# Kernel optimization log

Hardware: AMD Instinct MI355X
Metric: run time of the kernel (lower is better)

The kernel has to match this reference:

```python
import jax, jax.numpy as jnp
import numpy as np

EPS = 1e-5
N = 384
CZ = 128  # pair channels (c_z)
CH = 128  # hidden channels (c_hidden)


def _layer_norm(x, w, b):
    m = jnp.mean(x, axis=-1, keepdims=True)
    v = jnp.mean(jnp.square(x - m), axis=-1, keepdims=True)
    return (x - m) * jax.lax.rsqrt(v + EPS) * w + b


def setup_inputs() -> dict:
    key = jax.random.key(0)
    ks = jax.random.split(key, 8)
    s = 0.02  # weight init scale
    return {
        "z": jax.random.normal(ks[0], (1, N, N, CZ), jnp.float32),
        "ln_in_w": jnp.ones((2, CZ), jnp.float32),
        "ln_in_b": jnp.zeros((2, CZ), jnp.float32),
        "w_ag": jax.random.normal(ks[1], (2, CZ, CH), jnp.float32) * s,
        "b_ag": jnp.zeros((2, CH), jnp.float32),
        "w_ap": jax.random.normal(ks[2], (2, CZ, CH), jnp.float32) * s,
        "b_ap": jnp.zeros((2, CH), jnp.float32),
        "w_bg": jax.random.normal(ks[3], (2, CZ, CH), jnp.float32) * s,
        "b_bg": jnp.zeros((2, CH), jnp.float32),
        "w_bp": jax.random.normal(ks[4], (2, CZ, CH), jnp.float32) * s,
        "b_bp": jnp.zeros((2, CH), jnp.float32),
        "ln_out_w": jnp.ones((2, CH), jnp.float32),
        "ln_out_b": jnp.zeros((2, CH), jnp.float32),
        "w_z": jax.random.normal(ks[5], (2, CH, CZ), jnp.float32) * s,
        "b_z": jnp.zeros((2, CZ), jnp.float32),
        "w_g": jax.random.normal(ks[6], (2, CZ, CZ), jnp.float32) * s,
        "b_g": jnp.zeros((2, CZ), jnp.float32),
    }


def _tri_mul(z, outgoing, ln_in_w, ln_in_b, w_ag, b_ag, w_ap, b_ap,
             w_bg, b_bg, w_bp, b_bp, ln_out_w, ln_out_b, w_z, b_z, w_g, b_g):
    zn = _layer_norm(z, ln_in_w, ln_in_b)                      # [1,N,N,CZ]
    a = jax.nn.sigmoid(zn @ w_ag + b_ag) * (zn @ w_ap + b_ap)  # [1,N,N,CH]
    b = jax.nn.sigmoid(zn @ w_bg + b_bg) * (zn @ w_bp + b_bp)  # [1,N,N,CH]
    if outgoing:
        # p[i,k,c] = sum_j a[i,j,c] * b[k,j,c]
        p = jnp.einsum('bijc,bkjc->bikc', a, b)
    else:
        # p[i,k,c] = sum_j a[j,i,c] * b[j,k,c]
        p = jnp.einsum('bjic,bjkc->bikc', a, b)
    p = _layer_norm(p, ln_out_w, ln_out_b) @ w_z + b_z         # [1,N,N,CZ]
    g = jax.nn.sigmoid(zn @ w_g + b_g)
    return p * g


def reference(z, ln_in_w, ln_in_b, w_ag, b_ag, w_ap, b_ap, w_bg, b_bg,
              w_bp, b_bp, ln_out_w, ln_out_b, w_z, b_z, w_g, b_g):
    # idx 0: TriMulOut (outgoing=True), idx 1: TriMulIn (outgoing=False)
    for idx, outgoing in enumerate((True, False)):
        z = z + _tri_mul(z, outgoing,
                         ln_in_w[idx], ln_in_b[idx],
                         w_ag[idx], b_ag[idx], w_ap[idx], b_ap[idx],
                         w_bg[idx], b_bg[idx], w_bp[idx], b_bp[idx],
                         ln_out_w[idx], ln_out_b[idx],
                         w_z[idx], b_z[idx], w_g[idx], b_g[idx])
    return z
```

## Files before the change

### kernel.cpp

```cpp
#include <hip/hip_runtime.h>


constexpr int NS = 384;
constexpr int NN = NS * NS;

using bf16x8 = __attribute__((ext_vector_type(8))) __bf16;
using bf16x4 = __attribute__((ext_vector_type(4))) __bf16;
using f32x4  = __attribute__((ext_vector_type(4))) float;

__device__ inline void load16_to_lds(const __bf16* g, __bf16* lds) {
  auto* gp = reinterpret_cast<const __attribute__((address_space(1))) unsigned int*>(
      reinterpret_cast<uintptr_t>(g));
  auto* lp = reinterpret_cast<__attribute__((address_space(3))) unsigned int*>(
      reinterpret_cast<uintptr_t>(lds));
  __builtin_amdgcn_global_load_lds(gp, lp, 16, 0, 0);
}

__global__ __launch_bounds__(256) void prep_weights(
    const float* __restrict__ w_ag, const float* __restrict__ w_ap,
    const float* __restrict__ w_bg, const float* __restrict__ w_bp,
    const float* __restrict__ w_g,  const float* __restrict__ w_z,
    __bf16* __restrict__ wsw)
{
  int gid  = blockIdx.x * 256 + threadIdx.x;
  int mat  = gid >> 11;
  int slot = gid & 2047;
  int lane = slot & 63;
  int tb   = (slot >> 6) & 7;
  int s    = slot >> 9;
  int pass = mat / 6, which = mat % 6;
  const float* W;
  switch (which) {
    case 0: W = w_ag; break; case 1: W = w_ap; break; case 2: W = w_bg; break;
    case 3: W = w_bp; break; case 4: W = w_g;  break; default: W = w_z;
  }
  W += pass * 16384;
  int n0 = tb * 16 + (lane & 15);
  int k0 = s * 32 + (lane >> 4) * 8;
  __bf16* dst = wsw + ((size_t)mat * 2048 + slot) * 8;
#pragma unroll
  for (int j = 0; j < 8; ++j) dst[j] = (__bf16)W[(k0 + j) * 128 + n0];
}

__global__ __launch_bounds__(256) void proj_kernel(
    const float* __restrict__ zsrc, const float* __restrict__ lnw, const float* __restrict__ lnb,
    const __bf16* __restrict__ wsw5,
    const float* __restrict__ bag, const float* __restrict__ bap,
    const float* __restrict__ bbg, const float* __restrict__ bbp,
    __bf16* __restrict__ a_t, __bf16* __restrict__ b_t, int mode)
{
  __shared__ __bf16 zn[64][136];
  int tid = threadIdx.x;
  int rb = 0, r2 = 0;
  size_t pstart = 0;
  if (mode == 0) pstart = (size_t)blockIdx.x * 64;
  else { rb = blockIdx.x / NS; r2 = blockIdx.x % NS; }

  {
    int row = tid >> 2, q = tid & 3;
    size_t zoff = (mode == 0) ? (pstart + row) * 128
                              : ((size_t)(64 * rb + row) * NS + r2) * 128;
    const float4* zp = (const float4*)(zsrc + zoff) + q * 8;
    float4 v[8];
#pragma unroll
    for (int u = 0; u < 8; ++u) v[u] = zp[u];
    float s1 = 0.f, s2 = 0.f;
#pragma unroll
    for (int u = 0; u < 8; ++u) {
      float4 t = v[u];
      s1 += t.x + t.y + t.z + t.w;
      s2 += t.x * t.x + t.y * t.y + t.z * t.z + t.w * t.w;
    }
    s1 += __shfl_xor(s1, 1); s2 += __shfl_xor(s2, 1);
    s1 += __shfl_xor(s1, 2); s2 += __shfl_xor(s2, 2);
    float mean = s1 * (1.0f / 128.0f);
    float var  = s2 * (1.0f / 128.0f) - mean * mean;
    float rstd = rsqrtf(var + 1e-5f);
#pragma unroll
    for (int u = 0; u < 8; ++u) {
      int c0 = q * 32 + u * 4;
      float4 t  = v[u];
      float4 w4 = *(const float4*)(lnw + c0);
      float4 b4 = *(const float4*)(lnb + c0);
      zn[row][c0 + 0] = (__bf16)((t.x - mean) * rstd * w4.x + b4.x);
      zn[row][c0 + 1] = (__bf16)((t.y - mean) * rstd * w4.y + b4.y);
      zn[row][c0 + 2] = (__bf16)((t.z - mean) * rstd * w4.z + b4.z);
      zn[row][c0 + 3] = (__bf16)((t.w - mean) * rstd * w4.w + b4.w);
    }
  }
  __syncthreads();

  const int wv = tid >> 6;
  const int lane = tid & 63;
  const int lm = lane & 15;
  const int lq = lane >> 4;
  const size_t wposbase = (mode == 0) ? pstart : ((size_t)r2 * NS + 64 * rb);

  bf16x8 znf[4][4];
#pragma unroll
  for (int nt = 0; nt < 4; ++nt)
#pragma unroll
    for (int s = 0; s < 4; ++s)
      znf[nt][s] = *(const bf16x8*)(&zn[16 * nt + lm][32 * s + 8 * lq]);

#pragma unroll
  for (int grp = 0; grp < 2; ++grp) {
    const __bf16* wG = wsw5 + (size_t)(2 * grp) * 16384;
    const __bf16* wP = wG + 16384;
    const float* pg = grp ? bbg : bag;
    const float* pp = grp ? bbp : bap;
    __bf16* dst = grp ? b_t : a_t;

#pragma unroll
    for (int mbi = 0; mbi < 2; ++mbi) {
      const int mb = 2 * wv + mbi;
      bf16x8 fG[4], fP[4];
#pragma unroll
      for (int s = 0; s < 4; ++s) {
        fG[s] = *(const bf16x8*)(wG + ((size_t)((s * 8 + mb) * 64 + lane)) * 8);
        fP[s] = *(const bf16x8*)(wP + ((size_t)((s * 8 + mb) * 64 + lane)) * 8);
      }
      const int cc = 16 * mb + lm;
      float bG = pg[cc];
      float bP = pp[cc];
      __bf16* drow = dst + (size_t)cc * NN + wposbase + 4 * lq;
#pragma unroll
      for (int nt = 0; nt < 4; ++nt) {
        f32x4 acc0 = {0.f, 0.f, 0.f, 0.f}, acc1 = {0.f, 0.f, 0.f, 0.f};
#pragma unroll
        for (int s = 0; s < 4; ++s) {
          acc0 = __builtin_amdgcn_mfma_f32_16x16x32_bf16(znf[nt][s], fG[s], acc0, 0, 0, 0);
          acc1 = __builtin_amdgcn_mfma_f32_16x16x32_bf16(znf[nt][s], fP[s], acc1, 0, 0, 0);
        }
        bf16x4 pk;
#pragma unroll
        for (int r = 0; r < 4; ++r) {
          float xg = acc0[r] + bG;
          float xp = acc1[r] + bP;
          pk[r] = (__bf16)(xp / (1.0f + __expf(-xg)));
        }
        *(bf16x4*)(drow + 16 * nt) = pk;
      }
    }
  }
}

__global__ __launch_bounds__(256) void tri_kernel(
    const __bf16* __restrict__ a_t, const __bf16* __restrict__ b_t, __bf16* __restrict__ p_t)
{
  __shared__ __bf16 As[128 * 64];
  __shared__ __bf16 Bs[128 * 64];
  int c  = blockIdx.z;
  int i0 = blockIdx.x * 128, k0 = blockIdx.y * 128;
  const __bf16* Ab = a_t + (size_t)c * NN;
  const __bf16* Bb = b_t + (size_t)c * NN;
  int tid = threadIdx.x, wv = tid >> 6, lane = tid & 63;
  int lm = lane & 15, lq = lane >> 4;
  int lrow = lane >> 3;
  int lsl  = lane & 7;
  int lch  = lsl ^ lrow;
  f32x4 acc[4][4];
#pragma unroll
  for (int mi = 0; mi < 4; ++mi)
#pragma unroll
    for (int ni = 0; ni < 4; ++ni) acc[mi][ni] = {0.f, 0.f, 0.f, 0.f};
  const int rowA_half = 64 * (wv & 1), colB_half = 64 * (wv >> 1);

  for (int kk = 0; kk < 384; kk += 64) {
    __syncthreads();
#pragma unroll
    for (int v = 0; v < 4; ++v) {
      int rgrp = 4 * wv + v;
      int r = 8 * rgrp + lrow;
      load16_to_lds(Ab + (size_t)(i0 + r) * NS + kk + lch * 8, As + rgrp * 512);
      load16_to_lds(Bb + (size_t)(k0 + r) * NS + kk + lch * 8, Bs + rgrp * 512);
    }
    __syncthreads();
#pragma unroll
    for (int s = 0; s < 2; ++s) {
      bf16x8 bfr[4], afr[4];
#pragma unroll
      for (int ni = 0; ni < 4; ++ni)
        bfr[ni] = *(const bf16x8*)(Bs + (colB_half + 16 * ni + lm) * 64 +
                                   ((4 * s + lq) ^ (lm & 7)) * 8);
#pragma unroll
      for (int mi = 0; mi < 4; ++mi)
        afr[mi] = *(const bf16x8*)(As + (rowA_half + 16 * mi + lm) * 64 +
                                   ((4 * s + lq) ^ (lm & 7)) * 8);
#pragma unroll
      for (int mi = 0; mi < 4; ++mi)
#pragma unroll
        for (int ni = 0; ni < 4; ++ni)
          acc[mi][ni] = __builtin_amdgcn_mfma_f32_16x16x32_bf16(afr[mi], bfr[ni], acc[mi][ni], 0, 0, 0);
    }
  }
#pragma unroll
  for (int mi = 0; mi < 4; ++mi)
#pragma unroll
    for (int ni = 0; ni < 4; ++ni)
#pragma unroll
      for (int r = 0; r < 4; ++r) {
        int row = i0 + rowA_half + 16 * mi + 4 * lq + r;
        int col = k0 + colB_half + 16 * ni + lm;
        p_t[(size_t)c * NN + (size_t)row * NS + col] = (__bf16)acc[mi][ni][r];
      }
}

__global__ __launch_bounds__(256) void out_kernel(
    const __bf16* __restrict__ p_t,
    const float* __restrict__ z_in, float* __restrict__ z_out,
    const float* __restrict__ lniw, const float* __restrict__ lnib,
    const float* __restrict__ lnow, const float* __restrict__ lnob,
    const __bf16* __restrict__ wz, const float* __restrict__ bz,
    const __bf16* __restrict__ wg, const float* __restrict__ bg)
{
  __shared__ __bf16 pl[64][136];
  __shared__ __bf16 znl[64][136];
  int tid = threadIdx.x;
  size_t base = (size_t)blockIdx.x * 64;

  {
    int row = tid >> 2, q = tid & 3;
    const float4* zp = (const float4*)(z_in + (base + row) * 128) + q * 8;
    float4 v[8];
#pragma unroll
    for (int u = 0; u < 8; ++u) v[u] = zp[u];
    float s1 = 0.f, s2 = 0.f;
#pragma unroll
    for (int u = 0; u < 8; ++u) {
      float4 t = v[u];
      s1 += t.x + t.y + t.z + t.w;
      s2 += t.x * t.x + t.y * t.y + t.z * t.z + t.w * t.w;
    }
    s1 += __shfl_xor(s1, 1); s2 += __shfl_xor(s2, 1);
    s1 += __shfl_xor(s1, 2); s2 += __shfl_xor(s2, 2);
    float mean = s1 * (1.0f / 128.0f);
    float var  = s2 * (1.0f / 128.0f) - mean * mean;
    float rstd = rsqrtf(var + 1e-5f);
#pragma unroll
    for (int u = 0; u < 8; ++u) {
      int c0 = q * 32 + u * 4;
      float4 t  = v[u];
      float4 w4 = *(const float4*)(lniw + c0);
      float4 b4 = *(const float4*)(lnib + c0);
      znl[row][c0 + 0] = (__bf16)((t.x - mean) * rstd * w4.x + b4.x);
      znl[row][c0 + 1] = (__bf16)((t.y - mean) * rstd * w4.y + b4.y);
      znl[row][c0 + 2] = (__bf16)((t.z - mean) * rstd * w4.z + b4.z);
      znl[row][c0 + 3] = (__bf16)((t.w - mean) * rstd * w4.w + b4.w);
    }
  }

  {
    int c2 = tid >> 1, hf = tid & 1;
    const __bf16* src = p_t + (size_t)c2 * NN + base + hf * 32;
    bf16x8 v0 = ((const bf16x8*)src)[0];
    bf16x8 v1 = ((const bf16x8*)src)[1];
    bf16x8 v2 = ((const bf16x8*)src)[2];
    bf16x8 v3 = ((const bf16x8*)src)[3];
#pragma unroll
    for (int j = 0; j < 8; ++j) pl[hf * 32 + j][c2] = v0[j];
#pragma unroll
    for (int j = 0; j < 8; ++j) pl[hf * 32 + 8 + j][c2] = v1[j];
#pragma unroll
    for (int j = 0; j < 8; ++j) pl[hf * 32 + 16 + j][c2] = v2[j];
#pragma unroll
    for (int j = 0; j < 8; ++j) pl[hf * 32 + 24 + j][c2] = v3[j];
  }
  __syncthreads();

  {
    int row = tid >> 2, q = tid & 3;
    bf16x8 pv[4];
#pragma unroll
    for (int s = 0; s < 4; ++s) pv[s] = *(const bf16x8*)(&pl[row][q * 32 + 8 * s]);
    float s1 = 0.f, s2 = 0.f;
#pragma unroll
    for (int s = 0; s < 4; ++s)
#pragma unroll
      for (int j = 0; j < 8; ++j) { float f = (float)pv[s][j]; s1 += f; s2 += f * f; }
    s1 += __shfl_xor(s1, 1); s2 += __shfl_xor(s2, 1);
    s1 += __shfl_xor(s1, 2); s2 += __shfl_xor(s2, 2);
    float mean = s1 * (1.0f / 128.0f);
    float var  = s2 * (1.0f / 128.0f) - mean * mean;
    float rstd = rsqrtf(var + 1e-5f);
#pragma unroll
    for (int s = 0; s < 4; ++s) {
#pragma unroll
      for (int j = 0; j < 8; ++j) {
        int cc = q * 32 + 8 * s + j;
        float f = ((float)pv[s][j] - mean) * rstd * lnow[cc] + lnob[cc];
        pv[s][j] = (__bf16)f;
      }
      *(bf16x8*)(&pl[row][q * 32 + 8 * s]) = pv[s];
    }
  }
  __syncthreads();

  int wv = tid >> 6, lane = tid & 63, lm = lane & 15, lq = lane >> 4;
  bf16x8 wzf[2][4], wgf[2][4];
  float bzv[2], bgv[2];
#pragma unroll
  for (int nbi = 0; nbi < 2; ++nbi) {
    int nb = 2 * wv + nbi;
    bzv[nbi] = bz[16 * nb + lm];
    bgv[nbi] = bg[16 * nb + lm];
#pragma unroll
    for (int s = 0; s < 4; ++s) {
      wzf[nbi][s] = *(const bf16x8*)(wz + ((size_t)((s * 8 + nb) * 64 + lane)) * 8);
      wgf[nbi][s] = *(const bf16x8*)(wg + ((size_t)((s * 8 + nb) * 64 + lane)) * 8);
    }
  }
#pragma unroll
  for (int mt = 0; mt < 4; ++mt) {
    bf16x8 af[4], zf[4];
#pragma unroll
    for (int s = 0; s < 4; ++s) {
      af[s] = *(const bf16x8*)(&pl[16 * mt + lm][32 * s + 8 * lq]);
      zf[s] = *(const bf16x8*)(&znl[16 * mt + lm][32 * s + 8 * lq]);
    }
#pragma unroll
    for (int nbi = 0; nbi < 2; ++nbi) {
      f32x4 accp = {0.f, 0.f, 0.f, 0.f};
      f32x4 accg = {0.f, 0.f, 0.f, 0.f};
#pragma unroll
      for (int s = 0; s < 4; ++s) {
        accp = __builtin_amdgcn_mfma_f32_16x16x32_bf16(af[s], wzf[nbi][s], accp, 0, 0, 0);
        accg = __builtin_amdgcn_mfma_f32_16x16x32_bf16(zf[s], wgf[nbi][s], accg, 0, 0, 0);
      }
      int cz = 16 * (2 * wv + nbi) + lm;
#pragma unroll
      for (int r = 0; r < 4; ++r) {
        int pos = 16 * mt + 4 * lq + r;
        size_t idx = (base + pos) * 128 + cz;
        float gv  = 1.0f / (1.0f + __expf(-(accg[r] + bgv[nbi])));
        float res = (accp[r] + bzv[nbi]) * gv + z_in[idx];
        z_out[idx] = res;
      }
    }
  }
}

extern "C" void kernel_launch(void* const* d_in, const int* in_sizes, int n_in,
                              void* d_out, int out_size, void* d_ws, size_t ws_size,
                              hipStream_t stream) {
  (void)in_sizes; (void)n_in; (void)out_size; (void)ws_size;
  const float* z        = (const float*)d_in[0];
  const float* ln_in_w  = (const float*)d_in[1];
  const float* ln_in_b  = (const float*)d_in[2];
  const float* w_ag     = (const float*)d_in[3];
  const float* b_ag     = (const float*)d_in[4];
  const float* w_ap     = (const float*)d_in[5];
  const float* b_ap     = (const float*)d_in[6];
  const float* w_bg     = (const float*)d_in[7];
  const float* b_bg     = (const float*)d_in[8];
  const float* w_bp     = (const float*)d_in[9];
  const float* b_bp     = (const float*)d_in[10];
  const float* ln_out_w = (const float*)d_in[11];
  const float* ln_out_b = (const float*)d_in[12];
  const float* w_z      = (const float*)d_in[13];
  const float* b_z      = (const float*)d_in[14];
  const float* w_g      = (const float*)d_in[15];
  const float* b_g      = (const float*)d_in[16];
  float* out = (float*)d_out;

  __bf16* wsw = (__bf16*)d_ws;
  __bf16* a_t = wsw + 12 * 16384;
  __bf16* b_t = a_t + (size_t)NN * 128;
  __bf16* p_t = b_t + (size_t)NN * 128;

  prep_weights<<<96, 256, 0, stream>>>(w_ag, w_ap, w_bg, w_bp, w_g, w_z, wsw);

  for (int idx = 0; idx < 2; ++idx) {
    const float* zsrc = (idx == 0) ? z : out;
    const __bf16* wsw5 = wsw + (size_t)idx * 6 * 16384;
    proj_kernel<<<2304, 256, 0, stream>>>(
        zsrc, ln_in_w + idx * 128, ln_in_b + idx * 128, wsw5,
        b_ag + idx * 128, b_ap + idx * 128, b_bg + idx * 128, b_bp + idx * 128,
        a_t, b_t, idx);
    tri_kernel<<<dim3(3, 3, 128), 256, 0, stream>>>(a_t, b_t, p_t);
    out_kernel<<<2304, 256, 0, stream>>>(
        p_t, zsrc, out,
        ln_in_w + idx * 128, ln_in_b + idx * 128,
        ln_out_w + idx * 128, ln_out_b + idx * 128,
        wsw5 + 5 * 16384, b_z + idx * 128,
        wsw5 + 4 * 16384, b_g + idx * 128);
  }
}
```

Before: 451.2 us.

## Remap tri_kernel blocks per XCD, use rcp sigmoid, restructure proj fragment loads

The tri_kernel grid becomes a 1D launch whose block index is decoded so that all tiles of a channel land on the same XCD (block id mod 8), aiming for better L2 reuse of each channel's a/b slices. Sigmoid now uses the hardware v_rcp_f32 approximation instead of a full-precision divide, in both proj and out kernels. proj_kernel reloads zn fragments from LDS per set instead of holding a 4x4 register array, which lowers register pressure at the cost of repeated LDS reads. The approximate reciprocal slightly lowers precision.

```diff
diff --git a/kernel.cpp b/kernel.cpp
--- a/kernel.cpp
+++ b/kernel.cpp
@@ -14,6 +14,13 @@
   auto* lp = reinterpret_cast<__attribute__((address_space(3))) unsigned int*>(
       reinterpret_cast<uintptr_t>(lds));
   __builtin_amdgcn_global_load_lds(gp, lp, 16, 0, 0);
+}
+
+__device__ inline float fast_sigmoid(float x) {
+  float d = 1.0f + __expf(-x);
+  float r;
+  asm("v_rcp_f32 %0, %1" : "=v"(r) : "v"(d));
+  return r;
 }
 
 __global__ __launch_bounds__(256) void prep_weights(
@@ -56,6 +63,11 @@
   if (mode == 0) pstart = (size_t)blockIdx.x * 64;
   else { rb = blockIdx.x / NS; r2 = blockIdx.x % NS; }
 
+  const int wv = tid >> 6;
+  const int lane = tid & 63;
+  const int lm = lane & 15;
+  const int lq = lane >> 4;
+
   {
     int row = tid >> 2, q = tid & 3;
     size_t zoff = (mode == 0) ? (pstart + row) * 128
@@ -90,57 +102,48 @@
   }
   __syncthreads();
 
-  const int wv = tid >> 6;
-  const int lane = tid & 63;
-  const int lm = lane & 15;
-  const int lq = lane >> 4;
   const size_t wposbase = (mode == 0) ? pstart : ((size_t)r2 * NS + 64 * rb);
 
-  bf16x8 znf[4][4];
-#pragma unroll
-  for (int nt = 0; nt < 4; ++nt)
-#pragma unroll
-    for (int s = 0; s < 4; ++s)
-      znf[nt][s] = *(const bf16x8*)(&zn[16 * nt + lm][32 * s + 8 * lq]);
-
-#pragma unroll
-  for (int grp = 0; grp < 2; ++grp) {
+#pragma unroll
+  for (int set = 0; set < 4; ++set) {
+    const int grp = set >> 1, mbi = set & 1;
+    const int mb = 2 * wv + mbi;
     const __bf16* wG = wsw5 + (size_t)(2 * grp) * 16384;
     const __bf16* wP = wG + 16384;
-    const float* pg = grp ? bbg : bag;
-    const float* pp = grp ? bbp : bap;
+    bf16x8 fG[4], fP[4];
+#pragma unroll
+    for (int s = 0; s < 4; ++s) {
+      fG[s] = *(const bf16x8*)(wG + ((size_t)((s * 8 + mb) * 64 + lane)) * 8);
+      fP[s] = *(const bf16x8*)(wP + ((size_t)((s * 8 + mb) * 64 + lane)) * 8);
+    }
+    const int cc = 16 * mb + lm;
+    const float bG = (grp ? bbg : bag)[cc];
+    const float bP = (grp ? bbp : bap)[cc];
     __bf16* dst = grp ? b_t : a_t;
-
-#pragma unroll
-    for (int mbi = 0; mbi < 2; ++mbi) {
-      const int mb = 2 * wv + mbi;
-      bf16x8 fG[4], fP[4];
-#pragma unroll
-      for (int s = 0; s < 4; ++s) {
-        fG[s] = *(const bf16x8*)(wG + ((size_t)((s * 8 + mb) * 64 + lane)) * 8);
-        fP[s] = *(const bf16x8*)(wP + ((size_t)((s * 8 + mb) * 64 + lane)) * 8);
-      }
-      const int cc = 16 * mb + lm;
-      float bG = pg[cc];
-      float bP = pp[cc];
-      __bf16* drow = dst + (size_t)cc * NN + wposbase + 4 * lq;
-#pragma unroll
-      for (int nt = 0; nt < 4; ++nt) {
-        f32x4 acc0 = {0.f, 0.f, 0.f, 0.f}, acc1 = {0.f, 0.f, 0.f, 0.f};
-#pragma unroll
-        for (int s = 0; s < 4; ++s) {
-          acc0 = __builtin_amdgcn_mfma_f32_16x16x32_bf16(znf[nt][s], fG[s], acc0, 0, 0, 0);
-          acc1 = __builtin_amdgcn_mfma_f32_16x16x32_bf16(znf[nt][s], fP[s], acc1, 0, 0, 0);
-        }
-        bf16x4 pk;
-#pragma unroll
-        for (int r = 0; r < 4; ++r) {
-          float xg = acc0[r] + bG;
-          float xp = acc1[r] + bP;
-          pk[r] = (__bf16)(xp / (1.0f + __expf(-xg)));
-        }
-        *(bf16x4*)(drow + 16 * nt) = pk;
-      }
+    __bf16* drow = dst + (size_t)cc * NN + wposbase + 4 * lq;
+#pragma unroll
+    for (int nt = 0; nt < 4; ++nt) {
+      bf16x8 z0 = *(const bf16x8*)(&zn[16 * nt + lm][8 * lq]);
+      bf16x8 z1 = *(const bf16x8*)(&zn[16 * nt + lm][32 + 8 * lq]);
+      bf16x8 z2 = *(const bf16x8*)(&zn[16 * nt + lm][64 + 8 * lq]);
+      bf16x8 z3 = *(const bf16x8*)(&zn[16 * nt + lm][96 + 8 * lq]);
+      f32x4 acc0 = {0.f, 0.f, 0.f, 0.f}, acc1 = {0.f, 0.f, 0.f, 0.f};
+      acc0 = __builtin_amdgcn_mfma_f32_16x16x32_bf16(z0, fG[0], acc0, 0, 0, 0);
+      acc1 = __builtin_amdgcn_mfma_f32_16x16x32_bf16(z0, fP[0], acc1, 0, 0, 0);
+      acc0 = __builtin_amdgcn_mfma_f32_16x16x32_bf16(z1, fG[1], acc0, 0, 0, 0);
+      acc1 = __builtin_amdgcn_mfma_f32_16x16x32_bf16(z1, fP[1], acc1, 0, 0, 0);
+      acc0 = __builtin_amdgcn_mfma_f32_16x16x32_bf16(z2, fG[2], acc0, 0, 0, 0);
+      acc1 = __builtin_amdgcn_mfma_f32_16x16x32_bf16(z2, fP[2], acc1, 0, 0, 0);
+      acc0 = __builtin_amdgcn_mfma_f32_16x16x32_bf16(z3, fG[3], acc0, 0, 0, 0);
+      acc1 = __builtin_amdgcn_mfma_f32_16x16x32_bf16(z3, fP[3], acc1, 0, 0, 0);
+      bf16x4 pk;
+#pragma unroll
+      for (int r = 0; r < 4; ++r) {
+        float xg = acc0[r] + bG;
+        float xp = acc1[r] + bP;
+        pk[r] = (__bf16)(xp * fast_sigmoid(xg));
+      }
+      *(bf16x4*)(drow + 16 * nt) = pk;
     }
   }
 }
@@ -150,8 +153,13 @@
 {
   __shared__ __bf16 As[128 * 64];
   __shared__ __bf16 Bs[128 * 64];
-  int c  = blockIdx.z;
-  int i0 = blockIdx.x * 128, k0 = blockIdx.y * 128;
+  int lin = blockIdx.x;
+  int xcd = lin & 7;
+  int loc = lin >> 3;
+  int cq  = loc / 9;
+  int tile = loc - 9 * cq;
+  int c  = (xcd << 4) | cq;
+  int i0 = (tile % 3) * 128, k0 = (tile / 3) * 128;
   const __bf16* Ab = a_t + (size_t)c * NN;
   const __bf16* Bb = b_t + (size_t)c * NN;
   int tid = threadIdx.x, wv = tid >> 6, lane = tid & 63;
@@ -332,7 +340,7 @@
       for (int r = 0; r < 4; ++r) {
         int pos = 16 * mt + 4 * lq + r;
         size_t idx = (base + pos) * 128 + cz;
-        float gv  = 1.0f / (1.0f + __expf(-(accg[r] + bgv[nbi])));
+        float gv  = fast_sigmoid(accg[r] + bgv[nbi]);
         float res = (accp[r] + bzv[nbi]) * gv + z_in[idx];
         z_out[idx] = res;
       }
@@ -377,7 +385,7 @@
         zsrc, ln_in_w + idx * 128, ln_in_b + idx * 128, wsw5,
         b_ag + idx * 128, b_ap + idx * 128, b_bg + idx * 128, b_bp + idx * 128,
         a_t, b_t, idx);
-    tri_kernel<<<dim3(3, 3, 128), 256, 0, stream>>>(a_t, b_t, p_t);
+    tri_kernel<<<1152, 256, 0, stream>>>(a_t, b_t, p_t);
     out_kernel<<<2304, 256, 0, stream>>>(
         p_t, zsrc, out,
         ln_in_w + idx * 128, ln_in_b + idx * 128,
```

Measured after the change: 424.6 us. -5.9%, faster.
